# Kernel tuning notes

Measured on AMD Instinct MI355X. Metric: run time of the kernel, lower is better.

Reference implementation:

```python
import jax, jax.numpy as jnp
import numpy as np

DIM = 1024
HEAD_DIM = 64
CHUNK = 128
B, T = 4, 4096


def setup_inputs() -> dict:
    key = jax.random.key(0)
    ks = jax.random.split(key, 8)
    s = 1.0 / np.sqrt(DIM)
    inp = {
        'x': jax.random.normal(ks[0], (B, T, DIM), jnp.float32),
        'Wq': jax.random.normal(ks[1], (DIM, DIM), jnp.float32) * s,
        'bq': jnp.zeros((DIM,), jnp.float32),
        'Wk': jax.random.normal(ks[2], (DIM, DIM), jnp.float32) * s,
        'bk': jnp.zeros((DIM,), jnp.float32),
        'Wv': jax.random.normal(ks[3], (DIM, DIM), jnp.float32) * s,
        'bv': jnp.zeros((DIM,), jnp.float32),
        'Wbeta': jax.random.normal(ks[4], (DIM, DIM), jnp.float32) * s,
        'bbeta': jnp.zeros((DIM,), jnp.float32),
        'Walpha': jax.random.normal(ks[5], (DIM, DIM), jnp.float32) * s,
        'balpha': jnp.full((DIM,), 2.0, jnp.float32),  # bias init 2.0 as in torch
    }
    return inp


def reference(x, Wq, bq, Wk, bk, Wv, bv, Wbeta, bbeta, Walpha, balpha):
    Bsz, Tlen, D = x.shape
    d = HEAD_DIM
    H = D // d
    C = CHUNK
    scale = d ** (-0.5)

    q = ((x @ Wq.T + bq) * scale).reshape(Bsz, Tlen, H, d)
    k = ((x @ Wk.T + bk) * scale).reshape(Bsz, Tlen, H, d)
    v = (x @ Wv.T + bv).reshape(Bsz, Tlen, H, d)
    alpha_logits = jnp.clip((x @ Walpha.T + balpha).reshape(Bsz, Tlen, H, d), -10.0, 10.0)
    log_alpha = jax.nn.log_sigmoid(alpha_logits)
    alpha_val = jax.nn.sigmoid(alpha_logits)
    beta = jax.nn.softplus(x @ Wbeta.T + bbeta).reshape(Bsz, Tlen, H, d)

    # pad T to a multiple of C (static)
    pad = (-Tlen) % C
    if pad:
        pw = ((0, 0), (0, pad), (0, 0), (0, 0))
        q, k, v = jnp.pad(q, pw), jnp.pad(k, pw), jnp.pad(v, pw)
        log_alpha, beta = jnp.pad(log_alpha, pw), jnp.pad(beta, pw)
    N = q.shape[1] // C
    cshape = (Bsz, N, C, H, d)
    q, k, v = q.reshape(cshape), k.reshape(cshape), v.reshape(cshape)
    log_alpha, beta = log_alpha.reshape(cshape), beta.reshape(cshape)

    ccum = jnp.cumsum(log_alpha, axis=2)          # (B,N,C,H,d)
    m = ccum.mean(axis=-1)                        # (B,N,C,H); mean is linear -> take before pairwise diff
    decay_logits_mean = m[:, :, :, None, :] - m[:, :, None, :, :]  # (B,N,C,C,H)
    tril = jnp.tril(jnp.ones((C, C), jnp.float32))[None, None, :, :, None]
    decay_logits_mean = jnp.where(tril == 0, -1e9, decay_logits_mean)
    decay = jnp.exp(decay_logits_mean)            # (B,N,C,C,H)

    attn = jnp.einsum('bnihd,bnjhd->bnhij', q, k)
    attn = attn * decay.transpose(0, 1, 4, 2, 3)
    y_intra = jnp.einsum('bnhij,bnjhd->bnihd', attn, v * beta)  # (B,N,C,H,d)

    # inter-chunk recurrence via scan over chunks
    asum = jnp.exp(log_alpha.sum(axis=2).mean(axis=-1))  # (B,N,H) total chunk decay
    curve = jnp.exp(m)                                   # (B,N,C,H) intra-chunk decay curve
    bmean = beta.mean(axis=-1)                           # (B,N,C,H)

    def to_scan(a):
        return jnp.moveaxis(a, 1, 0)
    xs = (to_scan(q), to_scan(y_intra), to_scan(curve), to_scan(asum),
          to_scan(k), to_scan(v), to_scan(bmean))

    state0 = jnp.zeros((Bsz, H, d, d), jnp.float32)

    def step(state, inputs):
        qi, yi, ci, ai, ki, vi, bmi = inputs
        mem = jnp.einsum('bchq,bhqk->bchk', qi, state)
        y = yi + mem * ci[..., None]
        state = state * ai[:, :, None, None]
        delta = jnp.einsum('bchk,bchv,bch->bhkv', ki, vi, bmi)
        return state + delta, y

    state, ys = jax.lax.scan(step, state0, xs)
    y = jnp.moveaxis(ys, 0, 1).reshape(Bsz, N * C, D)
    if pad:
        y = y[:, :Tlen, :]
    return y, state, alpha_val
```

## Files before the change

### kernel.cpp

```cpp
#include <hip/hip_runtime.h>
#include <cstdint>
#include <cmath>

#define DIMM 1024
#define NHEAD 16
#define HEADD 64
#define CHUNKC 128
#define NBATCH 4
#define TLEN 4096
#define NCHUNK 32
#define BT (NBATCH * TLEN)
#define NSTACK (5 * DIMM)

typedef unsigned short ushort_t;
typedef __attribute__((ext_vector_type(8))) short short8;
typedef __attribute__((ext_vector_type(4))) float f32x4;

__device__ __forceinline__ float blo(unsigned int u) { return __uint_as_float(u << 16); }
__device__ __forceinline__ float bhi(unsigned int u) { return __uint_as_float(u & 0xffff0000u); }
__device__ __forceinline__ ushort_t f2bf(float f) {
  unsigned int u = __float_as_uint(f);
  u += 0x7fffu + ((u >> 16) & 1u);
  return (ushort_t)(u >> 16);
}
__device__ __forceinline__ float bf2f(ushort_t s) { return __uint_as_float(((unsigned int)s) << 16); }
__device__ __forceinline__ unsigned pack2(float a, float b) {
  return (unsigned)f2bf(a) | ((unsigned)f2bf(b) << 16);
}

__device__ __forceinline__ void async16(const ushort_t* g, ushort_t* l) {
  __builtin_amdgcn_global_load_lds((__attribute__((address_space(1))) void*)g,
                                   (__attribute__((address_space(3))) void*)l, 16, 0, 0);
}

__global__ __launch_bounds__(256) void k_cast(
    const float* __restrict__ x,
    const float* __restrict__ Wq, const float* __restrict__ Wk,
    const float* __restrict__ Wv, const float* __restrict__ Wb, const float* __restrict__ Wa,
    const float* __restrict__ bq, const float* __restrict__ bk,
    const float* __restrict__ bv, const float* __restrict__ bb, const float* __restrict__ ba,
    ushort_t* __restrict__ xb, ushort_t* __restrict__ wbm, float* __restrict__ bias_st) {
  const long XU = (long)BT * DIMM / 4;
  const long WU = (long)NSTACK * DIMM / 4;
  const long BU = NSTACK / 4;
  const long NU = XU + WU + BU;
  for (long u = (long)blockIdx.x * blockDim.x + threadIdx.x; u < NU;
       u += (long)gridDim.x * blockDim.x) {
    if (u < XU) {
      float4 f = ((const float4*)x)[u];
      ushort4 o;
      o.x = f2bf(f.x); o.y = f2bf(f.y); o.z = f2bf(f.z); o.w = f2bf(f.w);
      ((ushort4*)xb)[u] = o;
    } else if (u < XU + WU) {
      long j = u - XU;
      long e = j * 4;
      int row = (int)(e >> 10);
      int col = (int)(e & 1023);
      int p = row >> 10, wr = row & 1023;
      const float* Wp = (p == 0) ? Wq : (p == 1) ? Wk : (p == 2) ? Wv : (p == 3) ? Wb : Wa;
      float4 f = *(const float4*)(Wp + (size_t)wr * DIMM + col);
      ushort4 o;
      o.x = f2bf(f.x); o.y = f2bf(f.y); o.z = f2bf(f.z); o.w = f2bf(f.w);
      ((ushort4*)wbm)[j] = o;
    } else {
      long j = u - XU - WU;
      int e = (int)(j * 4);
      int p = e >> 10, r = e & 1023;
      const float* bp = (p == 0) ? bq : (p == 1) ? bk : (p == 2) ? bv : (p == 3) ? bb : ba;
      ((float4*)bias_st)[j] = *(const float4*)(bp + r);
    }
  }
}

__global__ __launch_bounds__(256) void k_proj(
    const ushort_t* __restrict__ xb, const ushort_t* __restrict__ wbm,
    const float* __restrict__ bias_st,
    ushort_t* __restrict__ qo, ushort_t* __restrict__ ko,
    ushort_t* __restrict__ vo, ushort_t* __restrict__ bo,
    float* __restrict__ ao) {
  __shared__ __align__(16) ushort_t smem[2 * 128 * 64];
  ushort_t* As = smem;
  ushort_t* Bs = smem + 128 * 64;
  const int tid = threadIdx.x;
  const int lane = tid & 63;
  const int wave = tid >> 6;
  const int quad = lane >> 4, lr = lane & 15;
  const int wr = (wave >> 1) * 64, wc = (wave & 1) * 64;
  const int sx = lr & 7;

  const int lid = blockIdx.y * 40 + blockIdx.x;
  const int swz = (lid & 7) * 640 + (lid >> 3);
  const int byn = swz / 40;
  const int bxn = swz - byn * 40;
  const int bm0 = byn * 128, bn0 = bxn * 128;

  const int trow = tid >> 3;
  const int gsw = ((tid & 7) ^ (trow & 7)) << 3;
  const ushort_t* agb = xb + (size_t)(bm0 + trow) * DIMM + gsw;
  const ushort_t* bgb = wbm + (size_t)(bn0 + trow) * DIMM + gsw;

  f32x4 zero = {0.f, 0.f, 0.f, 0.f};
  f32x4 acc[4][4];
#pragma unroll
  for (int i = 0; i < 4; ++i)
#pragma unroll
    for (int j = 0; j < 4; ++j) acc[i][j] = zero;

  for (int kk = 0; kk < DIMM; kk += 64) {
    __syncthreads();
#pragma unroll
    for (int c = 0; c < 4; ++c) {
      async16(agb + (size_t)(c * 32) * DIMM + kk, As + c * 2048 + tid * 8);
      async16(bgb + (size_t)(c * 32) * DIMM + kk, Bs + c * 2048 + tid * 8);
    }
    __syncthreads();
#pragma unroll
    for (int kh = 0; kh < 2; ++kh) {
      short8 af[4], bfr[4];
#pragma unroll
      for (int i = 0; i < 4; ++i)
        af[i] = *(const short8*)(As + (wr + i * 16 + lr) * 64 + (((kh * 4 + quad) ^ sx) << 3));
#pragma unroll
      for (int j = 0; j < 4; ++j)
        bfr[j] = *(const short8*)(Bs + (wc + j * 16 + lr) * 64 + (((kh * 4 + quad) ^ sx) << 3));
#pragma unroll
      for (int i = 0; i < 4; ++i)
#pragma unroll
        for (int j = 0; j < 4; ++j)
          acc[i][j] = __builtin_amdgcn_mfma_f32_16x16x32_bf16(af[i], bfr[j], acc[i][j], 0, 0, 0);
    }
  }

  const int p_id = bn0 >> 10;
  const int ncol0 = bn0 & 1023;

  if (p_id == 4) {
#pragma unroll
    for (int j = 0; j < 4; ++j) {
      const int colg = wc + j * 16 + lr;
      const float bias = bias_st[bn0 + colg];
      const int nc = ncol0 + colg;
#pragma unroll
      for (int i = 0; i < 4; ++i)
#pragma unroll
        for (int r = 0; r < 4; ++r) {
          const int rowl = wr + i * 16 + quad * 4 + r;
          float val = acc[i][j][r] + bias;
          float c = fminf(fmaxf(val, -10.f), 10.f);
          ao[(size_t)(bm0 + rowl) * DIMM + nc] = 1.f / (1.f + expf(-c));
        }
    }
  } else {
    ushort_t* outp = (p_id == 0) ? qo : (p_id == 1) ? ko : (p_id == 2) ? vo : bo;
    const float scl = (p_id <= 1) ? 0.125f : 1.f;
    ushort_t* T = smem;
    const int halfb = (wr == 64) ? 32 : 0;
#pragma unroll
    for (int pass = 0; pass < 2; ++pass) {
      __syncthreads();
#pragma unroll
      for (int ii = 0; ii < 2; ++ii) {
        const int i = pass * 2 + ii;
#pragma unroll
        for (int j = 0; j < 4; ++j) {
          const int col = wc + j * 16 + lr;
          const float bias = bias_st[bn0 + col];
#pragma unroll
          for (int r = 0; r < 4; ++r) {
            float val = acc[i][j][r] + bias;
            float ov;
            if (p_id == 3) ov = (val > 20.f) ? val : log1pf(expf(val));
            else ov = val * scl;
            T[(halfb + ii * 16 + quad * 4 + r) * 136 + col] = f2bf(ov);
          }
        }
      }
      __syncthreads();
      const int trw = tid >> 2;
      const int cch = (tid & 3) * 32;
      const int growl = pass * 32 + (trw & 31) + (trw >> 5) * 64;
      ushort_t* dst = outp + (size_t)(bm0 + growl) * DIMM + ncol0 + cch;
      const ushort_t* src = T + trw * 136 + cch;
#pragma unroll
      for (int u = 0; u < 4; ++u)
        *(uint4*)(dst + u * 8) = *(const uint4*)(src + u * 8);
    }
  }
}

__global__ __launch_bounds__(128) void k_stats(
    const float* __restrict__ alpha, const ushort_t* __restrict__ betaw,
    float* __restrict__ mArr, float* __restrict__ bmean, float* __restrict__ asum) {
  const int bnh = blockIdx.x;
  const int h = bnh & 15, n = (bnh >> 4) & 31, b = bnh >> 9;
  const int c = threadIdx.x;
  const size_t bt = (size_t)b * TLEN + n * CHUNKC + c;

  const float4* ap = (const float4*)(alpha + bt * DIMM + h * HEADD);
  float ls = 0.f;
#pragma unroll
  for (int w = 0; w < 16; ++w) {
    float4 a = ap[w];
    ls += logf(a.x) + logf(a.y) + logf(a.z) + logf(a.w);
  }
  const uint4* bp = (const uint4*)(betaw + bt * DIMM + h * HEADD);
  float bs = 0.f;
#pragma unroll
  for (int w = 0; w < 8; ++w) {
    uint4 u = bp[w];
    bs += blo(u.x) + bhi(u.x) + blo(u.y) + bhi(u.y) + blo(u.z) + bhi(u.z) + blo(u.w) + bhi(u.w);
  }
  float la = ls * (1.f / 64.f);

  __shared__ float s[128];
  s[c] = la;
  __syncthreads();
  for (int off = 1; off < 128; off <<= 1) {
    float t = (c >= off) ? s[c - off] : 0.f;
    __syncthreads();
    s[c] += t;
    __syncthreads();
  }
  float m = s[c];
  const size_t o = (size_t)bnh * CHUNKC + c;
  mArr[o] = m;
  bmean[o] = bs * (1.f / 64.f);
  if (c == 127) asum[bnh] = expf(m);
}

__global__ __launch_bounds__(256) void k_delta(
    const ushort_t* __restrict__ kw, const ushort_t* __restrict__ vw,
    const float* __restrict__ bmean, float* __restrict__ delta) {
  __shared__ ushort_t kc[8192];
  __shared__ ushort_t vc[8192];
  __shared__ float bm[128];
  const int bnh = blockIdx.x;
  const int h = bnh & 15, n = (bnh >> 4) & 31, b = bnh >> 9;
  const int tid = threadIdx.x;
  const size_t bt0 = (size_t)b * TLEN + n * CHUNKC;

#pragma unroll
  for (int it = 0; it < 4; ++it) {
    int u = tid + it * 256;
    int row = u >> 3, col = (u & 7) * 8;
    size_t go = (bt0 + row) * DIMM + h * HEADD + col;
    ((uint4*)kc)[u] = *(const uint4*)(kw + go);
    ((uint4*)vc)[u] = *(const uint4*)(vw + go);
  }
  if (tid < 128) bm[tid] = bmean[(size_t)bnh * CHUNKC + tid];
  __syncthreads();

  const int kd = tid >> 2, v0 = (tid & 3) * 16;
  float acc[16];
#pragma unroll
  for (int l = 0; l < 16; ++l) acc[l] = 0.f;

#pragma unroll 4
  for (int c = 0; c < 128; ++c) {
    float kb = bf2f(kc[c * 64 + kd]) * bm[c];
    const uint4* vr = (const uint4*)(vc + c * 64 + v0);
    uint4 u0 = vr[0], u1 = vr[1];
    acc[0] += kb * blo(u0.x);  acc[1] += kb * bhi(u0.x);
    acc[2] += kb * blo(u0.y);  acc[3] += kb * bhi(u0.y);
    acc[4] += kb * blo(u0.z);  acc[5] += kb * bhi(u0.z);
    acc[6] += kb * blo(u0.w);  acc[7] += kb * bhi(u0.w);
    acc[8] += kb * blo(u1.x);  acc[9] += kb * bhi(u1.x);
    acc[10] += kb * blo(u1.y); acc[11] += kb * bhi(u1.y);
    acc[12] += kb * blo(u1.z); acc[13] += kb * bhi(u1.z);
    acc[14] += kb * blo(u1.w); acc[15] += kb * bhi(u1.w);
  }
  float* dst = delta + (size_t)bnh * 4096 + kd * 64 + v0;
#pragma unroll
  for (int l4 = 0; l4 < 4; ++l4)
    ((float4*)dst)[l4] = make_float4(acc[l4 * 4], acc[l4 * 4 + 1], acc[l4 * 4 + 2], acc[l4 * 4 + 3]);
}

__global__ __launch_bounds__(256) void k_scan(
    const float* __restrict__ delta, const float* __restrict__ asum,
    float* __restrict__ Earr, float* __restrict__ state_out) {
  const int bh = blockIdx.x >> 4;
  const int g = blockIdx.x & 15;
  const int b = bh >> 4, h = bh & 15;
  const int elem = g * 256 + threadIdx.x;
  float e = 0.f;
  for (int n = 0; n < 32; ++n) {
    const size_t o = (((size_t)b * 32 + n) * 16 + h) * 4096 + elem;
    const float a = asum[((size_t)b * 32 + n) * 16 + h];
    Earr[o] = e;
    e = e * a + delta[o];
  }
  state_out[(size_t)bh * 4096 + elem] = e;
}

__global__ __launch_bounds__(256) void k_y(
    const ushort_t* __restrict__ qw, const ushort_t* __restrict__ kw,
    const ushort_t* __restrict__ vw, const ushort_t* __restrict__ betaw,
    const float* __restrict__ mArr, const float* __restrict__ Earr,
    float* __restrict__ yout) {
  __shared__ __align__(16) ushort_t vbt[64][200];
  __shared__ __align__(16) ushort_t pst[4][32][40];
  __shared__ float ms[128];
  const int bnh = blockIdx.x;
  const int h = bnh & 15, n = (bnh >> 4) & 31, b = bnh >> 9;
  const int tid = threadIdx.x;
  const int lane = tid & 63;
  const int wv = tid >> 6;
  const int quad = lane >> 4, lr = lane & 15;
  const int i0 = wv * 32;
  const size_t bt0 = (size_t)b * TLEN + n * CHUNKC;
  const size_t hoff = (size_t)h * HEADD;

#pragma unroll
  for (int it = 0; it < 4; ++it) {
    int u = tid + it * 256;
    int j = u & 127, vd0 = (u >> 7) * 8;
    size_t go = (bt0 + j) * DIMM + hoff + vd0;
    uint4 vv = *(const uint4*)(vw + go);
    uint4 bb2 = *(const uint4*)(betaw + go);
    vbt[vd0 + 0][j] = f2bf(blo(vv.x) * blo(bb2.x));
    vbt[vd0 + 1][j] = f2bf(bhi(vv.x) * bhi(bb2.x));
    vbt[vd0 + 2][j] = f2bf(blo(vv.y) * blo(bb2.y));
    vbt[vd0 + 3][j] = f2bf(bhi(vv.y) * bhi(bb2.y));
    vbt[vd0 + 4][j] = f2bf(blo(vv.z) * blo(bb2.z));
    vbt[vd0 + 5][j] = f2bf(bhi(vv.z) * bhi(bb2.z));
    vbt[vd0 + 6][j] = f2bf(blo(vv.w) * blo(bb2.w));
    vbt[vd0 + 7][j] = f2bf(bhi(vv.w) * bhi(bb2.w));
  }
  const float4* Eg = (const float4*)(Earr + (size_t)bnh * 4096);
#pragma unroll
  for (int it = 0; it < 4; ++it) {
    int u = tid + it * 256;
    int kd = u >> 4, vd0 = (u & 15) * 4;
    float4 ev = Eg[u];
    vbt[vd0 + 0][128 + kd] = f2bf(ev.x);
    vbt[vd0 + 1][128 + kd] = f2bf(ev.y);
    vbt[vd0 + 2][128 + kd] = f2bf(ev.z);
    vbt[vd0 + 3][128 + kd] = f2bf(ev.w);
  }
  if (tid < 128) ms[tid] = mArr[(size_t)bnh * CHUNKC + tid];
  __syncthreads();

  short8 qa[2][2];
#pragma unroll
  for (int it = 0; it < 2; ++it) {
    const ushort_t* qg = qw + (bt0 + i0 + it * 16 + lr) * DIMM + hoff + quad * 8;
    qa[it][0] = *(const short8*)(qg);
    qa[it][1] = *(const short8*)(qg + 32);
  }
  float mi[2][4];
#pragma unroll
  for (int it = 0; it < 2; ++it)
#pragma unroll
    for (int r = 0; r < 4; ++r) mi[it][r] = ms[i0 + it * 16 + quad * 4 + r];

  f32x4 zero = {0.f, 0.f, 0.f, 0.f};
  f32x4 acc2[2][4];
#pragma unroll
  for (int it = 0; it < 2; ++it)
#pragma unroll
    for (int nt = 0; nt < 4; ++nt) acc2[it][nt] = zero;

  for (int js = 0; js < 4; ++js) {
    const int j0 = js * 32;
#pragma unroll
    for (int jsub = 0; jsub < 2; ++jsub) {
      const int j0s = j0 + jsub * 16;
      const ushort_t* kg = kw + (bt0 + j0s + lr) * DIMM + hoff + quad * 8;
      short8 kb0 = *(const short8*)(kg);
      short8 kb1 = *(const short8*)(kg + 32);
      const float mj = ms[j0s + lr];
#pragma unroll
      for (int it = 0; it < 2; ++it) {
        f32x4 s = __builtin_amdgcn_mfma_f32_16x16x32_bf16(qa[it][0], kb0, zero, 0, 0, 0);
        s = __builtin_amdgcn_mfma_f32_16x16x32_bf16(qa[it][1], kb1, s, 0, 0, 0);
#pragma unroll
        for (int r = 0; r < 4; ++r) {
          const int ig = i0 + it * 16 + quad * 4 + r;
          const int jg = j0s + lr;
          float w = (jg > ig) ? 0.f : s[r] * __expf(mi[it][r] - mj);
          pst[wv][it * 16 + quad * 4 + r][jsub * 16 + lr] = f2bf(w);
        }
      }
    }
#pragma unroll
    for (int it = 0; it < 2; ++it) {
      short8 pa = *(const short8*)&pst[wv][it * 16 + lr][quad * 8];
#pragma unroll
      for (int nt = 0; nt < 4; ++nt) {
        short8 vb = *(const short8*)&vbt[nt * 16 + lr][j0 + quad * 8];
        acc2[it][nt] = __builtin_amdgcn_mfma_f32_16x16x32_bf16(pa, vb, acc2[it][nt], 0, 0, 0);
      }
    }
  }

#pragma unroll
  for (int es = 0; es < 2; ++es) {
    const int kd0 = es * 32;
    {
      const int row = lane >> 1;
      const int col0 = (lane & 1) * 16;
      const float ex = __expf(ms[i0 + row]);
      const ushort_t* qg = qw + (bt0 + i0 + row) * DIMM + hoff + kd0 + col0;
      uint4 u0 = *(const uint4*)(qg);
      uint4 u1 = *(const uint4*)(qg + 8);
      uint4 w0, w1;
      w0.x = pack2(blo(u0.x) * ex, bhi(u0.x) * ex);
      w0.y = pack2(blo(u0.y) * ex, bhi(u0.y) * ex);
      w0.z = pack2(blo(u0.z) * ex, bhi(u0.z) * ex);
      w0.w = pack2(blo(u0.w) * ex, bhi(u0.w) * ex);
      w1.x = pack2(blo(u1.x) * ex, bhi(u1.x) * ex);
      w1.y = pack2(blo(u1.y) * ex, bhi(u1.y) * ex);
      w1.z = pack2(blo(u1.z) * ex, bhi(u1.z) * ex);
      w1.w = pack2(blo(u1.w) * ex, bhi(u1.w) * ex);
      *(uint4*)&pst[wv][row][col0] = w0;
      *(uint4*)&pst[wv][row][col0 + 8] = w1;
    }
#pragma unroll
    for (int it = 0; it < 2; ++it) {
      short8 pa = *(const short8*)&pst[wv][it * 16 + lr][quad * 8];
#pragma unroll
      for (int nt = 0; nt < 4; ++nt) {
        short8 vb = *(const short8*)&vbt[nt * 16 + lr][128 + kd0 + quad * 8];
        acc2[it][nt] = __builtin_amdgcn_mfma_f32_16x16x32_bf16(pa, vb, acc2[it][nt], 0, 0, 0);
      }
    }
  }

#pragma unroll
  for (int it = 0; it < 2; ++it) {
#pragma unroll
    for (int nt = 0; nt < 4; ++nt) {
      f32x4 a = acc2[it][nt];
#pragma unroll
      for (int r = 0; r < 4; ++r) {
        const int ig = i0 + it * 16 + quad * 4 + r;
        yout[(bt0 + ig) * DIMM + hoff + nt * 16 + lr] = a[r];
      }
    }
  }
}

extern "C" void kernel_launch(void* const* d_in, const int* in_sizes, int n_in,
                              void* d_out, int out_size, void* d_ws, size_t ws_size,
                              hipStream_t stream) {
  const float* x  = (const float*)d_in[0];
  const float* Wq = (const float*)d_in[1];
  const float* bq = (const float*)d_in[2];
  const float* Wk = (const float*)d_in[3];
  const float* bk = (const float*)d_in[4];
  const float* Wv = (const float*)d_in[5];
  const float* bv = (const float*)d_in[6];
  const float* Wb = (const float*)d_in[7];
  const float* bb = (const float*)d_in[8];
  const float* Wa = (const float*)d_in[9];
  const float* ba = (const float*)d_in[10];

  char* ws = (char*)d_ws;
  ushort_t* xb   = (ushort_t*)(ws + 0);
  ushort_t* wbm  = (ushort_t*)(ws + 33554432);
  float* bias_st = (float*)(ws + 44040192);
  ushort_t* qw   = (ushort_t*)(ws + 44060672);
  ushort_t* kw   = (ushort_t*)(ws + 77615104);
  ushort_t* vw   = (ushort_t*)(ws + 111169536);
  ushort_t* bw   = (ushort_t*)(ws + 144723968);
  float* mArr    = (float*)(ws + 178278400);
  float* bmean   = (float*)(ws + 179326976);
  float* asum    = (float*)(ws + 180375552);
  float* delta   = (float*)(ws + 180383744);
  float* Earr    = (float*)(ws + 213938176);

  float* yout = (float*)d_out;
  float* state_out = yout + (size_t)BT * DIMM;
  float* aout = state_out + (size_t)NBATCH * NHEAD * 64 * 64;

  k_cast<<<dim3(4096), dim3(256), 0, stream>>>(x, Wq, Wk, Wv, Wb, Wa,
                                               bq, bk, bv, bb, ba, xb, wbm, bias_st);
  k_proj<<<dim3(40, 128), dim3(256), 0, stream>>>(xb, wbm, bias_st, qw, kw, vw, bw, aout);
  k_stats<<<dim3(2048), dim3(128), 0, stream>>>(aout, bw, mArr, bmean, asum);
  k_delta<<<dim3(2048), dim3(256), 0, stream>>>(kw, vw, bmean, delta);
  k_scan<<<dim3(1024), dim3(256), 0, stream>>>(delta, asum, Earr, state_out);
  k_y<<<dim3(2048), dim3(256), 0, stream>>>(qw, kw, vw, bw, mArr, Earr, yout);
}
```

Measured before the change: 677.6 us.

## Double-buffer projection GEMM LDS tiles with async prefetch of next K-slice

Restructures the projection GEMM main loop so the next 32-wide K tile is loaded into a second LDS buffer, using inline-asm global_load_lds with m0, while the current tile is consumed by MFMAs. This replaces the two barriers per 64-wide tile with one vmcnt wait plus barrier per step. It also changes the LDS XOR swizzle to suit the narrower tile and drops the block-index swizzle in favour of a plain grid mapping. The aim is to hide global-to-LDS load latency behind compute, at the cost of more loop iterations and possibly worse L2 locality without the block remap.

New measurement: 618.8 us. 1.09x faster.

```diff
diff --git a/kernel.cpp b/kernel.cpp
--- a/kernel.cpp
+++ b/kernel.cpp
@@ -28,9 +28,11 @@
   return (unsigned)f2bf(a) | ((unsigned)f2bf(b) << 16);
 }
 
-__device__ __forceinline__ void async16(const ushort_t* g, ushort_t* l) {
-  __builtin_amdgcn_global_load_lds((__attribute__((address_space(1))) void*)g,
-                                   (__attribute__((address_space(3))) void*)l, 16, 0, 0);
+__device__ __forceinline__ void stage16(unsigned lds_base, const ushort_t* g) {
+  asm volatile("s_mov_b32 m0, %0\n\t"
+               "global_load_lds_dwordx4 %1, off"
+               :: "s"(lds_base), "v"((unsigned long long)(size_t)g)
+               : "memory");
 }
 
 __global__ __launch_bounds__(256) void k_cast(
@@ -72,32 +74,41 @@
   }
 }
 
+#define BARR __builtin_amdgcn_s_barrier()
+#define VMC0 asm volatile("s_waitcnt vmcnt(0)" ::: "memory")
+
+#define STAGEP(bb, kt) do {                                                      \
+    const size_t _ko = (size_t)(kt) * 32;                                        \
+    unsigned _base = (unsigned)__builtin_amdgcn_readfirstlane(                   \
+        (int)(unsigned)(size_t)((__attribute__((address_space(3))) char*)smem    \
+                                + (bb) * 16384 + wv1024));                       \
+    stage16(_base,         agb + _ko);                                           \
+    stage16(_base + 4096,  agb + (size_t)64 * DIMM + _ko);                       \
+    stage16(_base + 8192,  bgb + _ko);                                           \
+    stage16(_base + 12288, bgb + (size_t)64 * DIMM + _ko);                       \
+  } while (0)
+
 __global__ __launch_bounds__(256) void k_proj(
     const ushort_t* __restrict__ xb, const ushort_t* __restrict__ wbm,
     const float* __restrict__ bias_st,
     ushort_t* __restrict__ qo, ushort_t* __restrict__ ko,
     ushort_t* __restrict__ vo, ushort_t* __restrict__ bo,
     float* __restrict__ ao) {
-  __shared__ __align__(16) ushort_t smem[2 * 128 * 64];
-  ushort_t* As = smem;
-  ushort_t* Bs = smem + 128 * 64;
+  __shared__ __align__(16) char smem[32768];
   const int tid = threadIdx.x;
   const int lane = tid & 63;
   const int wave = tid >> 6;
   const int quad = lane >> 4, lr = lane & 15;
   const int wr = (wave >> 1) * 64, wc = (wave & 1) * 64;
-  const int sx = lr & 7;
-
-  const int lid = blockIdx.y * 40 + blockIdx.x;
-  const int swz = (lid & 7) * 640 + (lid >> 3);
-  const int byn = swz / 40;
-  const int bxn = swz - byn * 40;
-  const int bm0 = byn * 128, bn0 = bxn * 128;
-
-  const int trow = tid >> 3;
-  const int gsw = ((tid & 7) ^ (trow & 7)) << 3;
-  const ushort_t* agb = xb + (size_t)(bm0 + trow) * DIMM + gsw;
-  const ushort_t* bgb = wbm + (size_t)(bn0 + trow) * DIMM + gsw;
+  const int sx = (lr >> 1) & 3;
+  const int wv1024 = wave * 1024;
+
+  const int bm0 = blockIdx.y * 128, bn0 = blockIdx.x * 128;
+
+  const int trow = tid >> 2;
+  const int gcol = (((tid & 3) ^ ((tid >> 3) & 3)) << 3);
+  const ushort_t* agb = xb + (size_t)(bm0 + trow) * DIMM + gcol;
+  const ushort_t* bgb = wbm + (size_t)(bn0 + trow) * DIMM + gcol;
 
   f32x4 zero = {0.f, 0.f, 0.f, 0.f};
   f32x4 acc[4][4];
@@ -106,29 +117,27 @@
 #pragma unroll
     for (int j = 0; j < 4; ++j) acc[i][j] = zero;
 
-  for (int kk = 0; kk < DIMM; kk += 64) {
-    __syncthreads();
-#pragma unroll
-    for (int c = 0; c < 4; ++c) {
-      async16(agb + (size_t)(c * 32) * DIMM + kk, As + c * 2048 + tid * 8);
-      async16(bgb + (size_t)(c * 32) * DIMM + kk, Bs + c * 2048 + tid * 8);
-    }
-    __syncthreads();
-#pragma unroll
-    for (int kh = 0; kh < 2; ++kh) {
-      short8 af[4], bfr[4];
-#pragma unroll
-      for (int i = 0; i < 4; ++i)
-        af[i] = *(const short8*)(As + (wr + i * 16 + lr) * 64 + (((kh * 4 + quad) ^ sx) << 3));
+  STAGEP(0, 0);
+
+#pragma unroll 2
+  for (int kk = 0; kk < 32; ++kk) {
+    VMC0;
+    BARR;
+    if (kk < 31) STAGEP((kk + 1) & 1, kk + 1);
+    const char* Ab = smem + (kk & 1) * 16384;
+    const char* Bb = Ab + 8192;
+    short8 af[4], bfr[4];
+#pragma unroll
+    for (int i = 0; i < 4; ++i)
+      af[i] = *(const short8*)(Ab + (wr + i * 16 + lr) * 64 + ((quad ^ sx) << 4));
+#pragma unroll
+    for (int j = 0; j < 4; ++j)
+      bfr[j] = *(const short8*)(Bb + (wc + j * 16 + lr) * 64 + ((quad ^ sx) << 4));
+#pragma unroll
+    for (int i = 0; i < 4; ++i)
 #pragma unroll
       for (int j = 0; j < 4; ++j)
-        bfr[j] = *(const short8*)(Bs + (wc + j * 16 + lr) * 64 + (((kh * 4 + quad) ^ sx) << 3));
-#pragma unroll
-      for (int i = 0; i < 4; ++i)
-#pragma unroll
-        for (int j = 0; j < 4; ++j)
-          acc[i][j] = __builtin_amdgcn_mfma_f32_16x16x32_bf16(af[i], bfr[j], acc[i][j], 0, 0, 0);
-    }
+        acc[i][j] = __builtin_amdgcn_mfma_f32_16x16x32_bf16(af[i], bfr[j], acc[i][j], 0, 0, 0);
   }
 
   const int p_id = bn0 >> 10;
@@ -153,7 +162,7 @@
   } else {
     ushort_t* outp = (p_id == 0) ? qo : (p_id == 1) ? ko : (p_id == 2) ? vo : bo;
     const float scl = (p_id <= 1) ? 0.125f : 1.f;
-    ushort_t* T = smem;
+    ushort_t* T = (ushort_t*)smem;
     const int halfb = (wr == 64) ? 32 : 0;
 #pragma unroll
     for (int pass = 0; pass < 2; ++pass) {
@@ -187,6 +196,10 @@
     }
   }
 }
+
+#undef STAGEP
+#undef BARR
+#undef VMC0
 
 __global__ __launch_bounds__(128) void k_stats(
     const float* __restrict__ alpha, const ushort_t* __restrict__ betaw,
```
